# Optimization experiments

Hardware: AMD Instinct MI355X
Metric: run time of the kernel (lower is better)

Reference implementation:

```python
import jax, jax.numpy as jnp
import numpy as np

N = 36          # number of independent LSTM streams (input_dim)
H = 256         # hidden units
G = 4 * H       # gate width (i, f, g, o)
SPEC = 6
OUT = 30
B, T = 32, 128


def setup_inputs() -> dict:
    key = jax.random.key(0)
    ks = jax.random.split(key, 18)
    s = 0.05
    d = {}
    d["x"] = jax.random.normal(ks[0], (B, T, N), dtype=jnp.float32)
    d["spec"] = jax.random.normal(ks[1], (B, SPEC), dtype=jnp.float32)
    # 36 stacked 2-layer LSTMs, batched along leading stream axis N.
    # Layer 1: input_size=1, so W_ih collapses to [N, G].
    d["Wih1"] = jax.random.normal(ks[2], (N, G), dtype=jnp.float32) * s
    d["Whh1"] = jax.random.normal(ks[3], (N, G, H), dtype=jnp.float32) * s
    d["bih1"] = jax.random.normal(ks[4], (N, G), dtype=jnp.float32) * s
    d["bhh1"] = jax.random.normal(ks[5], (N, G), dtype=jnp.float32) * s
    # Layer 2: input_size=H.
    d["Wih2"] = jax.random.normal(ks[6], (N, G, H), dtype=jnp.float32) * s
    d["Whh2"] = jax.random.normal(ks[7], (N, G, H), dtype=jnp.float32) * s
    d["bih2"] = jax.random.normal(ks[8], (N, G), dtype=jnp.float32) * s
    d["bhh2"] = jax.random.normal(ks[9], (N, G), dtype=jnp.float32) * s
    # spec_dense: Linear(6, H); stored as [in, out].
    d["Wspec"] = jax.random.normal(ks[10], (SPEC, H), dtype=jnp.float32) * s
    d["bspec"] = jax.random.normal(ks[11], (H,), dtype=jnp.float32) * s
    # predicter: Linear(H*(N+1), H) -> ReLU -> Linear(H, OUT); stored as [in, out].
    d["Wp1"] = jax.random.normal(ks[12], (H * (N + 1), H), dtype=jnp.float32) * s
    d["bp1"] = jax.random.normal(ks[13], (H,), dtype=jnp.float32) * s
    d["Wp2"] = jax.random.normal(ks[14], (H, OUT), dtype=jnp.float32) * s
    d["bp2"] = jax.random.normal(ks[15], (OUT,), dtype=jnp.float32) * s
    return d


def _lstm_cell(gates, c):
    # torch gate order: input, forget, cell(g), output
    i, f, g, o = jnp.split(gates, 4, axis=-1)
    c = jax.nn.sigmoid(f) * c + jax.nn.sigmoid(i) * jnp.tanh(g)
    h = jax.nn.sigmoid(o) * jnp.tanh(c)
    return h, c


def reference(x, spec, Wih1, Whh1, bih1, bhh1, Wih2, Whh2, bih2, bhh2,
              Wspec, bspec, Wp1, bp1, Wp2, bp2):
    b = x.shape[0]
    bg1 = bih1 + bhh1  # [N, G]
    bg2 = bih2 + bhh2

    def step(carry, x_t):
        # x_t: [B, N] scalar input per stream at this timestep
        h1, c1, h2, c2 = carry
        g1 = x_t[:, :, None] * Wih1[None] + jnp.einsum('bnh,ngh->bng', h1, Whh1) + bg1
        h1, c1 = _lstm_cell(g1, c1)
        g2 = (jnp.einsum('bnh,ngh->bng', h1, Wih2)
              + jnp.einsum('bnh,ngh->bng', h2, Whh2) + bg2)
        h2, c2 = _lstm_cell(g2, c2)
        return (h1, c1, h2, c2), None

    z = jnp.zeros((b, N, H), x.dtype)
    (h1, c1, h2, c2), _ = jax.lax.scan(step, (z, z, z, z), jnp.transpose(x, (1, 0, 2)))
    hidden_all = h2.reshape(b, N * H)          # concat of last-step top-layer h per stream
    hidden_spec = spec @ Wspec + bspec         # [B, H]
    feat = jnp.concatenate([hidden_all, hidden_spec], axis=1)  # [B, (N+1)*H]
    return jax.nn.relu(feat @ Wp1 + bp1) @ Wp2 + bp2
```

## Files before the change

### kernel.cpp

```cpp
#include <hip/hip_runtime.h>
#include <cstdint>
#include <cstddef>


constexpr int kN = 36, kH = 256, kG = 1024, kB = 32, kT = 128, kSpec = 6, kOut = 30;
constexpr int kHP = 264;
constexpr int kD1 = 16;

typedef __bf16 bf16;
typedef __bf16 bf16x8 __attribute__((ext_vector_type(8)));
typedef float f32x4 __attribute__((ext_vector_type(4)));
typedef unsigned long long u64;
typedef unsigned int u32;

__device__ __forceinline__ float sigm(float v) { return 1.f / (1.f + __expf(-v)); }
__device__ __forceinline__ float tanh_f(float v) {
  v = fminf(15.f, fmaxf(-15.f, v));
  float e = __expf(2.f * v);
  return (e - 1.f) / (e + 1.f);
}
__device__ __forceinline__ unsigned short f2bf(float f) {
  bf16 b = (bf16)f;
  return __builtin_bit_cast(unsigned short, b);
}
__device__ __forceinline__ u64 pload(const u64* p) {
  return __hip_atomic_load(p, __ATOMIC_RELAXED, __HIP_MEMORY_SCOPE_AGENT);
}
__device__ __forceinline__ void pstore(u64* p, u64 v) {
  __hip_atomic_store(p, v, __ATOMIC_RELAXED, __HIP_MEMORY_SCOPE_AGENT);
}
__device__ __forceinline__ u32 pload32(const u32* p) {
  return __hip_atomic_load(p, __ATOMIC_RELAXED, __HIP_MEMORY_SCOPE_AGENT);
}
__device__ __forceinline__ void pstore32(u32* p, u32 v) {
  __hip_atomic_store(p, v, __ATOMIC_RELAXED, __HIP_MEMORY_SCOPE_AGENT);
}


__device__ __forceinline__ void issue16(const u64* __restrict__ base, int tid, u64* v) {
#pragma unroll
  for (int i = 0; i < 16; ++i) v[i] = pload(base + (size_t)i * 256 + tid);
}
__device__ __forceinline__ void finish16(const u64* __restrict__ base, u32 want,
                                         int tid, u64* v) {
  u32 got = 0;
  for (;;) {
#pragma unroll
    for (int i = 0; i < 16; ++i)
      if (!(got & (1u << i)) && (u32)(v[i] >> 32) == want) got |= 1u << i;
    if (got == 0xFFFFu) return;
#pragma unroll
    for (int i = 0; i < 16; ++i)
      if (!(got & (1u << i))) v[i] = pload(base + (size_t)i * 256 + tid);
  }
}
__device__ __forceinline__ void poll16_stage(const u64* __restrict__ base, u32 want,
                                             int tid, unsigned short (*hs)[kHP]) {
  u64 v[16];
  u32 got = 0;
#pragma unroll
  for (int i = 0; i < 16; ++i) v[i] = pload(base + (size_t)i * 256 + tid);
  for (;;) {
#pragma unroll
    for (int i = 0; i < 16; ++i) {
      if (!(got & (1u << i)) && (u32)(v[i] >> 32) == want) {
        got |= 1u << i;
        hs[i][tid] = (unsigned short)v[i];
        hs[i + 16][tid] = (unsigned short)(v[i] >> 16);
      }
    }
    if (got == 0xFFFFu) return;
#pragma unroll
    for (int i = 0; i < 16; ++i)
      if (!(got & (1u << i))) v[i] = pload(base + (size_t)i * 256 + tid);
  }
}
__device__ __forceinline__ void poll8_stage(const u64* __restrict__ base, u32 want,
                                            int tid, int pc0, unsigned short (*hs)[kHP]) {
  const int c = pc0 + (tid & 127), m0 = (tid >> 7) * 8;
  u64 v[8];
  u32 got = 0;
#pragma unroll
  for (int i = 0; i < 8; ++i) v[i] = pload(base + (size_t)(m0 + i) * 256 + c);
  for (;;) {
#pragma unroll
    for (int i = 0; i < 8; ++i) {
      if (!(got & (1u << i)) && (u32)(v[i] >> 32) == want) {
        got |= 1u << i;
        hs[m0 + i][c] = (unsigned short)v[i];
        hs[m0 + i + 16][c] = (unsigned short)(v[i] >> 16);
      }
    }
    if (got == 0xFFu) return;
#pragma unroll
    for (int i = 0; i < 8; ++i)
      if (!(got & (1u << i))) v[i] = pload(base + (size_t)(m0 + i) * 256 + c);
  }
}

__global__ __launch_bounds__(256) void k_convert(
    const float* __restrict__ wa, const float* __restrict__ wb, const float* __restrict__ wc,
    bf16* __restrict__ oa, bf16* __restrict__ ob, bf16* __restrict__ oc)
{
  const size_t total = (size_t)kN * 64 * 8 * 64;
  size_t gid = (size_t)blockIdx.x * 256 + threadIdx.x;
  if (gid >= total) return;
  const int lane = (int)(gid & 63);
  const int ks = (int)((gid >> 6) & 7);
  const int nt = (int)((gid >> 9) & 63);
  const int n = (int)(gid >> 15);
  const int g = nt * 16 + (lane & 15);
  const int k = ks * 32 + (lane >> 4) * 8;
  const size_t so = ((size_t)n * kG + g) * kH + k;

  const float4 a0 = *(const float4*)(wa + so), a1 = *(const float4*)(wa + so + 4);
  const float4 b0 = *(const float4*)(wb + so), b1 = *(const float4*)(wb + so + 4);
  const float4 c0 = *(const float4*)(wc + so), c1 = *(const float4*)(wc + so + 4);
  bf16x8 va, vb, vc;
  va[0]=(bf16)a0.x; va[1]=(bf16)a0.y; va[2]=(bf16)a0.z; va[3]=(bf16)a0.w;
  va[4]=(bf16)a1.x; va[5]=(bf16)a1.y; va[6]=(bf16)a1.z; va[7]=(bf16)a1.w;
  vb[0]=(bf16)b0.x; vb[1]=(bf16)b0.y; vb[2]=(bf16)b0.z; vb[3]=(bf16)b0.w;
  vb[4]=(bf16)b1.x; vb[5]=(bf16)b1.y; vb[6]=(bf16)b1.z; vb[7]=(bf16)b1.w;
  vc[0]=(bf16)c0.x; vc[1]=(bf16)c0.y; vc[2]=(bf16)c0.z; vc[3]=(bf16)c0.w;
  vc[4]=(bf16)c1.x; vc[5]=(bf16)c1.y; vc[6]=(bf16)c1.z; vc[7]=(bf16)c1.w;
  ((bf16x8*)oa)[gid] = va;
  ((bf16x8*)ob)[gid] = vb;
  ((bf16x8*)oc)[gid] = vc;
}

__global__ __launch_bounds__(256) __attribute__((amdgpu_waves_per_eu(1, 1)))
void k_lstm(
    const float* __restrict__ x, const float* __restrict__ Wih1,
    const float* __restrict__ bih1, const float* __restrict__ bhh1,
    const float* __restrict__ bih2, const float* __restrict__ bhh2,
    const bf16* __restrict__ pk1, const bf16* __restrict__ pk2i,
    const bf16* __restrict__ pk2h, float* __restrict__ h2_final,
    u64* __restrict__ h1r, u64* __restrict__ h2r, u32* __restrict__ prog)
{
  const int blk = blockIdx.x;
  const int tid = threadIdx.x, wv = tid >> 6, lane = tid & 63;
  const int l15 = lane & 15, l4 = lane >> 4;

  __shared__ alignas(16) unsigned short hs1[kB][kHP];

  if (blk < 72) {
    const int n = blk >> 1, j = blk & 1;
    __shared__ float xsh[kT][kB];
    for (int i = tid; i < kB * kT; i += 256) {
      int b = i >> 7, t = i & 127;
      xsh[t][b] = x[((size_t)b * kT + t) * kN + n];
    }
    bf16x8 W[2][4][8];
    {
      const bf16x8* base = (const bf16x8*)pk1 + (size_t)n * 32768;
#pragma unroll
      for (int jj = 0; jj < 2; ++jj)
#pragma unroll
        for (int gt = 0; gt < 4; ++gt)
#pragma unroll
          for (int ks = 0; ks < 8; ++ks)
            W[jj][gt][ks] = base[(size_t)(gt * 16 + j * 8 + wv * 2 + jj) * 512 + ks * 64 + lane];
    }
    float wih[2][4], bg[2][4];
#pragma unroll
    for (int jj = 0; jj < 2; ++jj)
#pragma unroll
      for (int gt = 0; gt < 4; ++gt) {
        int g = gt * 256 + j * 128 + wv * 32 + jj * 16 + l15;
        wih[jj][gt] = Wih1[n * kG + g];
        bg[jj][gt] = bih1[n * kG + g] + bhh1[n * kG + g];
      }
    float cst[2][2][4];
#pragma unroll
    for (int a = 0; a < 2; ++a)
#pragma unroll
      for (int b = 0; b < 2; ++b)
#pragma unroll
        for (int r = 0; r < 4; ++r) cst[a][b][r] = 0.f;

    u64* ringn = h1r + (size_t)n * kD1 * 4096;
    u32* pg = prog + n * 4;
    const int pc0 = (1 - j) * 128, myb = j * 128 + wv * 32;
    __syncthreads();

#pragma unroll 1
    for (int t = 0; t < kT; ++t) {
      if ((t & 7) == 0 && t) {
        if (tid == 0) {
          for (;;) {
            u32 m0 = pload32(&pg[0]), m1 = pload32(&pg[1]);
            u32 m2 = pload32(&pg[2]), m3 = pload32(&pg[3]);
            u32 mn = m0 < m1 ? m0 : m1;
            mn = mn < m2 ? mn : m2;
            mn = mn < m3 ? mn : m3;
            if ((int)mn + 8 >= t) break;
          }
        }
        __syncthreads();
      }
      f32x4 acc[2][2][4];
#pragma unroll
      for (int mt = 0; mt < 2; ++mt)
#pragma unroll
        for (int jj = 0; jj < 2; ++jj)
#pragma unroll
          for (int gt = 0; gt < 4; ++gt)
#pragma unroll
            for (int r = 0; r < 4; ++r)
              acc[mt][jj][gt][r] = xsh[t][mt * 16 + l4 * 4 + r] * wih[jj][gt] + bg[jj][gt];
      if (t > 0) {
        poll8_stage(ringn + (size_t)((t - 1) % kD1) * 4096, (u32)t, tid, pc0, hs1);
        __syncthreads();
#pragma unroll
        for (int ks = 0; ks < 8; ++ks) {
          bf16x8 A0 = *(const bf16x8*)&hs1[l15][ks * 32 + l4 * 8];
          bf16x8 A1 = *(const bf16x8*)&hs1[16 + l15][ks * 32 + l4 * 8];
#pragma unroll
          for (int jj = 0; jj < 2; ++jj)
#pragma unroll
            for (int gt = 0; gt < 4; ++gt) {
              acc[0][jj][gt] = __builtin_amdgcn_mfma_f32_16x16x32_bf16(A0, W[jj][gt][ks], acc[0][jj][gt], 0, 0, 0);
              acc[1][jj][gt] = __builtin_amdgcn_mfma_f32_16x16x32_bf16(A1, W[jj][gt][ks], acc[1][jj][gt], 0, 0, 0);
            }
        }
      }
      float hv[2][2][4];
#pragma unroll
      for (int mt = 0; mt < 2; ++mt)
#pragma unroll
        for (int jj = 0; jj < 2; ++jj)
#pragma unroll
          for (int r = 0; r < 4; ++r) {
            float cc = sigm(acc[mt][jj][1][r]) * cst[mt][jj][r]
                     + sigm(acc[mt][jj][0][r]) * tanh_f(acc[mt][jj][2][r]);
            cst[mt][jj][r] = cc;
            hv[mt][jj][r] = sigm(acc[mt][jj][3][r]) * tanh_f(cc);
          }
      u64* pub = ringn + (size_t)(t % kD1) * 4096;
      const u64 tagw = ((u64)(u32)(t + 1)) << 32;
#pragma unroll
      for (int jj = 0; jj < 2; ++jj)
#pragma unroll
        for (int r = 0; r < 4; ++r) {
          int c = myb + jj * 16 + l15, m = l4 * 4 + r;
          pstore(&pub[(size_t)m * 256 + c],
                 tagw | ((u64)f2bf(hv[1][jj][r]) << 16) | f2bf(hv[0][jj][r]));
        }
#pragma unroll
      for (int mt = 0; mt < 2; ++mt)
#pragma unroll
        for (int jj = 0; jj < 2; ++jj)
#pragma unroll
          for (int r = 0; r < 4; ++r)
            hs1[mt * 16 + l4 * 4 + r][myb + jj * 16 + l15] = f2bf(hv[mt][jj][r]);
    }
  } else {
    const int bb = blk - 72, n = bb >> 2, q = bb & 3;
    __shared__ alignas(16) unsigned short hs2[kB][kHP];

    bf16x8 Wi[4][8], Wh[4][8];
    {
      const bf16x8* bi = (const bf16x8*)pk2i + (size_t)n * 32768;
      const bf16x8* bh = (const bf16x8*)pk2h + (size_t)n * 32768;
#pragma unroll
      for (int gt = 0; gt < 4; ++gt)
#pragma unroll
        for (int ks = 0; ks < 8; ++ks) {
          size_t o = (size_t)(gt * 16 + q * 4 + wv) * 512 + ks * 64 + lane;
          Wi[gt][ks] = bi[o];
          Wh[gt][ks] = bh[o];
        }
    }
    const int col = q * 64 + wv * 16 + l15;
    float bg[4];
#pragma unroll
    for (int gt = 0; gt < 4; ++gt) {
      int g = gt * 256 + col;
      bg[gt] = bih2[n * kG + g] + bhh2[n * kG + g];
    }
    float cst[2][4];
#pragma unroll
    for (int mt = 0; mt < 2; ++mt)
#pragma unroll
      for (int r = 0; r < 4; ++r) cst[mt][r] = 0.f;

    u64* ringn = h1r + (size_t)n * kD1 * 4096;
    u64* h2n = h2r + (size_t)n * 2 * 4096;
    u32* pg = prog + n * 4 + q;
    __syncthreads();

    u64 v1[16];
    issue16(ringn, tid, v1);
    finish16(ringn, 1u, tid, v1);

#pragma unroll 1
    for (int t = 0; t < kT; ++t) {
#pragma unroll
      for (int i = 0; i < 16; ++i) {
        hs1[i][tid] = (unsigned short)v1[i];
        hs1[i + 16][tid] = (unsigned short)(v1[i] >> 16);
      }
      __syncthreads();
      if (tid == 0) pstore32(pg, (u32)(t + 1));
      const u64* pn = ringn + (size_t)((t + 1) % kD1) * 4096;
      if (t + 1 < kT) issue16(pn, tid, v1);
      f32x4 acc[2][4];
#pragma unroll
      for (int mt = 0; mt < 2; ++mt)
#pragma unroll
        for (int gt = 0; gt < 4; ++gt)
#pragma unroll
          for (int r = 0; r < 4; ++r) acc[mt][gt][r] = bg[gt];
#pragma unroll
      for (int ks = 0; ks < 8; ++ks) {
        bf16x8 A0 = *(const bf16x8*)&hs1[l15][ks * 32 + l4 * 8];
        bf16x8 A1 = *(const bf16x8*)&hs1[16 + l15][ks * 32 + l4 * 8];
#pragma unroll
        for (int gt = 0; gt < 4; ++gt) {
          acc[0][gt] = __builtin_amdgcn_mfma_f32_16x16x32_bf16(A0, Wi[gt][ks], acc[0][gt], 0, 0, 0);
          acc[1][gt] = __builtin_amdgcn_mfma_f32_16x16x32_bf16(A1, Wi[gt][ks], acc[1][gt], 0, 0, 0);
        }
      }
      if (t > 0) {
        poll16_stage(h2n + (size_t)((t - 1) & 1) * 4096, (u32)t, tid, hs2);
        __syncthreads();
#pragma unroll
        for (int ks = 0; ks < 8; ++ks) {
          bf16x8 A0 = *(const bf16x8*)&hs2[l15][ks * 32 + l4 * 8];
          bf16x8 A1 = *(const bf16x8*)&hs2[16 + l15][ks * 32 + l4 * 8];
#pragma unroll
          for (int gt = 0; gt < 4; ++gt) {
            acc[0][gt] = __builtin_amdgcn_mfma_f32_16x16x32_bf16(A0, Wh[gt][ks], acc[0][gt], 0, 0, 0);
            acc[1][gt] = __builtin_amdgcn_mfma_f32_16x16x32_bf16(A1, Wh[gt][ks], acc[1][gt], 0, 0, 0);
          }
        }
      }
      float hv[2][4];
#pragma unroll
      for (int mt = 0; mt < 2; ++mt)
#pragma unroll
        for (int r = 0; r < 4; ++r) {
          float cc = sigm(acc[mt][1][r]) * cst[mt][r]
                   + sigm(acc[mt][0][r]) * tanh_f(acc[mt][2][r]);
          cst[mt][r] = cc;
          hv[mt][r] = sigm(acc[mt][3][r]) * tanh_f(cc);
        }
      u64* pub = h2n + (size_t)(t & 1) * 4096;
      const u64 tagw = ((u64)(u32)(t + 1)) << 32;
#pragma unroll
      for (int r = 0; r < 4; ++r) {
        int m = l4 * 4 + r;
        pstore(&pub[(size_t)m * 256 + col],
               tagw | ((u64)f2bf(hv[1][r]) << 16) | f2bf(hv[0][r]));
      }
      if (t == kT - 1) {
#pragma unroll
        for (int mt = 0; mt < 2; ++mt)
#pragma unroll
          for (int r = 0; r < 4; ++r)
            h2_final[((size_t)n * kB + (mt * 16 + l4 * 4 + r)) * kH + col] = hv[mt][r];
      }
      if (t + 1 < kT) finish16(pn, (u32)(t + 2), tid, v1);
      __syncthreads();
    }
  }
}

__global__ __launch_bounds__(256) void k_head1(
    const float* __restrict__ spec, const float* __restrict__ Wspec,
    const float* __restrict__ bspec, const float* __restrict__ Wp1,
    const float* __restrict__ h2f, float* __restrict__ partial)
{
  const int kc = blockIdx.x;
  const int b = blockIdx.y;
  const int o = threadIdx.x;
  __shared__ float fs[kH];
  if (kc < kN) {
    fs[o] = h2f[((size_t)kc * kB + b) * kH + o];
  } else {
    float v = bspec[o];
#pragma unroll
    for (int s = 0; s < kSpec; ++s) v += spec[b * kSpec + s] * Wspec[s * kH + o];
    fs[o] = v;
  }
  __syncthreads();
  const float* __restrict__ wp = Wp1 + (size_t)kc * 256 * kH + o;
  float a = 0.f;
#pragma unroll 8
  for (int i = 0; i < 256; ++i) a += fs[i] * wp[(size_t)i * kH];
  partial[((size_t)kc * kB + b) * kH + o] = a;
}

__global__ __launch_bounds__(256) void k_head2(
    const float* __restrict__ bp1, const float* __restrict__ Wp2,
    const float* __restrict__ bp2, const float* __restrict__ partial,
    float* __restrict__ out)
{
  const int b = blockIdx.x;
  const int o = threadIdx.x;
  __shared__ float hid[kH];
  float a = bp1[o];
#pragma unroll
  for (int kc = 0; kc < kN + 1; ++kc) a += partial[((size_t)kc * kB + b) * kH + o];
  hid[o] = fmaxf(a, 0.f);
  __syncthreads();
  if (o < kOut) {
    float r = bp2[o];
#pragma unroll 8
    for (int h = 0; h < kH; ++h) r += hid[h] * Wp2[h * kOut + o];
    out[b * kOut + o] = r;
  }
}

extern "C" void kernel_launch(void* const* d_in, const int* in_sizes, int n_in,
                              void* d_out, int out_size, void* d_ws, size_t ws_size,
                              hipStream_t stream) {
  const float* x = (const float*)d_in[0];
  const float* spec = (const float*)d_in[1];
  const float* Wih1 = (const float*)d_in[2];
  const float* Whh1 = (const float*)d_in[3];
  const float* bih1 = (const float*)d_in[4];
  const float* bhh1 = (const float*)d_in[5];
  const float* Wih2 = (const float*)d_in[6];
  const float* Whh2 = (const float*)d_in[7];
  const float* bih2 = (const float*)d_in[8];
  const float* bhh2 = (const float*)d_in[9];
  const float* Wspec = (const float*)d_in[10];
  const float* bspec = (const float*)d_in[11];
  const float* Wp1 = (const float*)d_in[12];
  const float* bp1 = (const float*)d_in[13];
  const float* Wp2 = (const float*)d_in[14];
  const float* bp2 = (const float*)d_in[15];
  float* out = (float*)d_out;

  const size_t WSZ = (size_t)kN * kG * kH;
  u32* prog = (u32*)d_ws;
  u64* h1r = (u64*)((char*)d_ws + 4096);
  u64* h2r = h1r + (size_t)kN * kD1 * 4096;
  bf16* pk1 = (bf16*)(h2r + (size_t)kN * 2 * 4096);
  bf16* pk2i = pk1 + WSZ;
  bf16* pk2h = pk2i + WSZ;
  float* h2_final = (float*)(pk2h + WSZ);
  float* partial = h2_final + (size_t)kN * kB * kH;

  hipMemsetAsync(d_ws, 0, 4096, stream);

  const size_t groups = (size_t)kN * 64 * 8 * 64;
  k_convert<<<dim3((unsigned)((groups + 255) / 256)), dim3(256), 0, stream>>>(
      Whh1, Wih2, Whh2, pk1, pk2i, pk2h);
  k_lstm<<<dim3(216), dim3(256), 0, stream>>>(
      x, Wih1, bih1, bhh1, bih2, bhh2, pk1, pk2i, pk2h, h2_final, h1r, h2r, prog);
  k_head1<<<dim3(kN + 1, kB), dim3(256), 0, stream>>>(spec, Wspec, bspec, Wp1, h2_final, partial);
  k_head2<<<dim3(kB), dim3(256), 0, stream>>>(bp1, Wp2, bp2, partial, out);
}
```

Baseline: 875.1 us.

## Overlap ring polling with partial MFMA work and use fast reciprocal activations

Splits the layer-1 recurrent MFMA into two halves. The half whose hidden columns this block produced itself is computed while loads from the partner block's ring slot are in flight, and the remaining half runs after the poll completes. Layer-2 blocks now issue the h2 ring loads before the input-side MFMAs so that load latency is hidden. Sigmoid and tanh switch to a hardware reciprocal form without clamping, which may change accuracy slightly. An extra __syncthreads at the end of each layer-1 step adds a barrier to protect the shared buffer reuse.

```diff
diff --git a/kernel.cpp b/kernel.cpp
--- a/kernel.cpp
+++ b/kernel.cpp
@@ -13,11 +13,10 @@
 typedef unsigned long long u64;
 typedef unsigned int u32;
 
-__device__ __forceinline__ float sigm(float v) { return 1.f / (1.f + __expf(-v)); }
+__device__ __forceinline__ float rcpf(float v) { return __builtin_amdgcn_rcpf(v); }
+__device__ __forceinline__ float sigm(float v) { return rcpf(1.f + __expf(-v)); }
 __device__ __forceinline__ float tanh_f(float v) {
-  v = fminf(15.f, fmaxf(-15.f, v));
-  float e = __expf(2.f * v);
-  return (e - 1.f) / (e + 1.f);
+  return fmaf(-2.f, rcpf(1.f + __expf(2.f * v)), 1.f);
 }
 __device__ __forceinline__ unsigned short f2bf(float f) {
   bf16 b = (bf16)f;
@@ -54,12 +53,10 @@
       if (!(got & (1u << i))) v[i] = pload(base + (size_t)i * 256 + tid);
   }
 }
-__device__ __forceinline__ void poll16_stage(const u64* __restrict__ base, u32 want,
-                                             int tid, unsigned short (*hs)[kHP]) {
-  u64 v[16];
+__device__ __forceinline__ void finish16_stage(const u64* __restrict__ base, u32 want,
+                                               int tid, unsigned short (*hs)[kHP],
+                                               u64* v) {
   u32 got = 0;
-#pragma unroll
-  for (int i = 0; i < 16; ++i) v[i] = pload(base + (size_t)i * 256 + tid);
   for (;;) {
 #pragma unroll
     for (int i = 0; i < 16; ++i) {
@@ -75,13 +72,17 @@
       if (!(got & (1u << i))) v[i] = pload(base + (size_t)i * 256 + tid);
   }
 }
-__device__ __forceinline__ void poll8_stage(const u64* __restrict__ base, u32 want,
-                                            int tid, int pc0, unsigned short (*hs)[kHP]) {
+__device__ __forceinline__ void issue8h(const u64* __restrict__ base, int tid, int pc0,
+                                        u64* v) {
   const int c = pc0 + (tid & 127), m0 = (tid >> 7) * 8;
-  u64 v[8];
+#pragma unroll
+  for (int i = 0; i < 8; ++i) v[i] = pload(base + (size_t)(m0 + i) * 256 + c);
+}
+__device__ __forceinline__ void finish8_stage(const u64* __restrict__ base, u32 want,
+                                              int tid, int pc0,
+                                              unsigned short (*hs)[kHP], u64* v) {
+  const int c = pc0 + (tid & 127), m0 = (tid >> 7) * 8;
   u32 got = 0;
-#pragma unroll
-  for (int i = 0; i < 8; ++i) v[i] = pload(base + (size_t)(m0 + i) * 256 + c);
   for (;;) {
 #pragma unroll
     for (int i = 0; i < 8; ++i) {
@@ -128,6 +129,23 @@
   ((bf16x8*)oc)[gid] = vc;
 }
 
+#define L1_MFMA_HALF(KS0)                                                            \
+  _Pragma("unroll")                                                                  \
+  for (int kk = 0; kk < 4; ++kk) {                                                   \
+    const int ks = (KS0) + kk;                                                       \
+    bf16x8 A0 = *(const bf16x8*)&hs1[l15][ks * 32 + l4 * 8];                         \
+    bf16x8 A1 = *(const bf16x8*)&hs1[16 + l15][ks * 32 + l4 * 8];                    \
+    _Pragma("unroll")                                                                \
+    for (int jj = 0; jj < 2; ++jj)                                                   \
+      _Pragma("unroll")                                                              \
+      for (int gt = 0; gt < 4; ++gt) {                                               \
+        acc[0][jj][gt] = __builtin_amdgcn_mfma_f32_16x16x32_bf16(                    \
+            A0, W[jj][gt][ks], acc[0][jj][gt], 0, 0, 0);                             \
+        acc[1][jj][gt] = __builtin_amdgcn_mfma_f32_16x16x32_bf16(                    \
+            A1, W[jj][gt][ks], acc[1][jj][gt], 0, 0, 0);                             \
+      }                                                                              \
+  }
+
 __global__ __launch_bounds__(256) __attribute__((amdgpu_waves_per_eu(1, 1)))
 void k_lstm(
     const float* __restrict__ x, const float* __restrict__ Wih1,
@@ -209,20 +227,13 @@
             for (int r = 0; r < 4; ++r)
               acc[mt][jj][gt][r] = xsh[t][mt * 16 + l4 * 4 + r] * wih[jj][gt] + bg[jj][gt];
       if (t > 0) {
-        poll8_stage(ringn + (size_t)((t - 1) % kD1) * 4096, (u32)t, tid, pc0, hs1);
+        const u64* ps = ringn + (size_t)((t - 1) % kD1) * 4096;
+        u64 pv[8];
+        issue8h(ps, tid, pc0, pv);
+        if (j == 0) { L1_MFMA_HALF(0) } else { L1_MFMA_HALF(4) }
+        finish8_stage(ps, (u32)t, tid, pc0, hs1, pv);
         __syncthreads();
-#pragma unroll
-        for (int ks = 0; ks < 8; ++ks) {
-          bf16x8 A0 = *(const bf16x8*)&hs1[l15][ks * 32 + l4 * 8];
-          bf16x8 A1 = *(const bf16x8*)&hs1[16 + l15][ks * 32 + l4 * 8];
-#pragma unroll
-          for (int jj = 0; jj < 2; ++jj)
-#pragma unroll
-            for (int gt = 0; gt < 4; ++gt) {
-              acc[0][jj][gt] = __builtin_amdgcn_mfma_f32_16x16x32_bf16(A0, W[jj][gt][ks], acc[0][jj][gt], 0, 0, 0);
-              acc[1][jj][gt] = __builtin_amdgcn_mfma_f32_16x16x32_bf16(A1, W[jj][gt][ks], acc[1][jj][gt], 0, 0, 0);
-            }
-        }
+        if (j == 0) { L1_MFMA_HALF(4) } else { L1_MFMA_HALF(0) }
       }
       float hv[2][2][4];
 #pragma unroll
@@ -253,6 +264,7 @@
 #pragma unroll
           for (int r = 0; r < 4; ++r)
             hs1[mt * 16 + l4 * 4 + r][myb + jj * 16 + l15] = f2bf(hv[mt][jj][r]);
+      __syncthreads();
     }
   } else {
     const int bb = blk - 72, n = bb >> 2, q = bb & 3;
@@ -304,6 +316,9 @@
       if (tid == 0) pstore32(pg, (u32)(t + 1));
       const u64* pn = ringn + (size_t)((t + 1) % kD1) * 4096;
       if (t + 1 < kT) issue16(pn, tid, v1);
+      u64 v2[16];
+      const u64* p2 = h2n + (size_t)((t - 1) & 1) * 4096;
+      if (t > 0) issue16(p2, tid, v2);
       f32x4 acc[2][4];
 #pragma unroll
       for (int mt = 0; mt < 2; ++mt)
@@ -322,7 +337,7 @@
         }
       }
       if (t > 0) {
-        poll16_stage(h2n + (size_t)((t - 1) & 1) * 4096, (u32)t, tid, hs2);
+        finish16_stage(p2, (u32)t, tid, hs2, v2);
         __syncthreads();
 #pragma unroll
         for (int ks = 0; ks < 8; ++ks) {
```

Result: slower. 903.9 us (+3.3%).
